# Kernel tuning notes

Hardware: AMD Instinct MI355X
Metric: run time of the kernel (lower is better)

## Reference

```python
import jax, jax.numpy as jnp
import numpy as np

B, L, DM, DI, N = 8, 2048, 512, 768, 8  # batch, seq, d_model, d_inner=int(1.5*512), d_state


def setup_inputs() -> dict:
    key = jax.random.key(0)
    ks = jax.random.split(key, 8)
    g = lambda k, shape, sc=1.0: (jax.random.normal(k, shape, jnp.float32) * sc)
    return {
        "x": g(ks[0], (B, L, DM)),
        "W_in": g(ks[1], (DM, 2 * DI), 0.02),    # in_proj weight (stored in->out)
        "A_log": g(ks[2], (DI, N)),               # nn.Parameter(randn)
        "D_param": g(ks[3], (DI,)),               # skip-connection D
        "W_x": g(ks[4], (DI, N), 0.02),           # x_proj weight
        "W_dt": g(ks[5], (N, DI), 0.02),          # dt_proj weight
        "b_dt": jnp.zeros((DI,), jnp.float32),    # dt_proj bias
        "W_out": g(ks[6], (DI, DM), 0.02),        # out_proj weight
    }


def reference(x, W_in, A_log, D_param, W_x, W_dt, b_dt, W_out):
    xz = x @ W_in                                  # (B,L,2*DI)
    d_inner = W_in.shape[1] // 2
    x_ssm, z = xz[..., :d_inner], xz[..., d_inner:]
    x_ssm = jax.nn.silu(x_ssm)                     # (B,L,DI)
    A = -jnp.exp(A_log.astype(jnp.float32))        # (DI,N)
    delta = jax.nn.softplus((x_ssm @ W_x) @ W_dt + b_dt)  # (B,L,DI)

    n_state = A.shape[-1]

    def step(h, inp):
        xt, dt = inp                               # each (B,DI)
        dA = jnp.exp(dt[..., None] * A)            # (B,DI,N)
        h = dA * h + dt[..., None] * xt[..., None]
        y = jnp.sum(h, axis=-1) + D_param * xt     # (B,DI)
        return h, y

    h0 = jnp.zeros((x.shape[0], d_inner, n_state), x_ssm.dtype)
    xs = (jnp.swapaxes(x_ssm, 0, 1), jnp.swapaxes(delta, 0, 1))  # (L,B,DI)
    _, ys = jax.lax.scan(step, h0, xs)             # ys: (L,B,DI)
    y = jnp.swapaxes(ys, 0, 1)                     # (B,L,DI)
    y = y * jax.nn.silu(z)
    return y @ W_out                               # (B,L,DM)
```

## Files before the change

### kernel.cpp

```cpp
#include <hip/hip_runtime.h>

typedef unsigned short bfu;
typedef __attribute__((ext_vector_type(8))) short short8;
typedef __attribute__((ext_vector_type(4))) float f32x4;

__device__ __forceinline__ float bf2f(bfu u){
  union { unsigned int i; float f; } v; v.i = ((unsigned int)u) << 16; return v.f;
}
__device__ __forceinline__ bfu f2bf(float f){
  union { float f; unsigned int i; } v; v.f = f;
  unsigned int r = (v.i + 0x7FFFu + ((v.i >> 16) & 1u)) >> 16;
  return (bfu)r;
}
__device__ __forceinline__ float fexp2(float x){ return __builtin_amdgcn_exp2f(x); }
__device__ __forceinline__ float flog2(float x){ return __builtin_amdgcn_logf(x); }
__device__ __forceinline__ float softplusf(float x){
  float t = fexp2(-fabsf(x) * 1.44269504088896f);
  return fmaxf(x, 0.f) + 0.69314718055995f * flog2(1.f + t);
}
__device__ __forceinline__ void gload16(const bfu* g, bfu* l){
  __builtin_amdgcn_global_load_lds((const __attribute__((address_space(1))) unsigned int*)g,
                                   (__attribute__((address_space(3))) unsigned int*)l, 16, 0, 0);
}

__global__ __launch_bounds__(256) void cvt_all_kernel(const float* __restrict__ x, bfu* __restrict__ x_bf,
                                                      const float* __restrict__ W_in, const float* __restrict__ W_out,
                                                      const float* __restrict__ W_x,
                                                      bfu* __restrict__ WinT, bfu* __restrict__ WoutT,
                                                      float* __restrict__ WxT){
  int g = blockIdx.x * 256 + threadIdx.x;
  if (g < 2097152){
    float4 v = ((const float4*)x)[g];
    ushort4 o;
    o.x = f2bf(v.x); o.y = f2bf(v.y); o.z = f2bf(v.z); o.w = f2bf(v.w);
    ((ushort4*)x_bf)[g] = o;
    return;
  }
  int h = g - 2097152;
  if (h < 786432){
    int r = h % 512, c = h / 512;
    WinT[h] = f2bf(W_in[(size_t)r * 1536 + c]);
  } else if (h < 786432 + 393216){
    int h2 = h - 786432;
    int r = h2 % 768, c = h2 / 768;
    WoutT[h2] = f2bf(W_out[(size_t)r * 512 + c]);
  } else if (h < 786432 + 393216 + 6144){
    int h2 = h - (786432 + 393216);
    int n = h2 / 768, k = h2 % 768;
    WxT[h2] = W_x[(size_t)k * 8 + n];
  }
}

template<int EPI, int KK>
__global__ __launch_bounds__(512)
void gemm_2p(const bfu* __restrict__ Amat, const bfu* __restrict__ Bt,
             void* __restrict__ out0, void* __restrict__ out1,
             int NBN, int N)
{
  constexpr int NT = KK / 64;
  __shared__ bfu LDS[2 * 24576];
  const int tid  = threadIdx.x;
  const int lane = tid & 63;
  const int w    = tid >> 6;
  const int wr   = w >> 1, wc = w & 1;

  const int cpx = gridDim.x >> 3;
  const int id  = blockIdx.x;
  const int nid = (id & 7) * cpx + (id >> 3);
  const int bn  = nid % NBN;
  const int bm  = nid / NBN;

  const int srow = tid >> 3;
  const int scol = ((tid & 7) ^ (srow & 7)) * 8;
  const bfu* gA = Amat + ((size_t)(bm * 256 + srow)) * KK + scol;
  const bfu* gB = Bt   + ((size_t)(bn * 128 + srow)) * KK + scol;

  auto STAGE = [&](int t, int buf){
    const int k0 = t * 64;
    bfu* dst = (bfu*)LDS + buf * 24576 + tid * 8;
    #pragma unroll
    for (int i = 0; i < 4; i++)
      gload16(gA + (size_t)(i * 64) * KK + k0, dst + i * 4096);
    #pragma unroll
    for (int j = 0; j < 2; j++)
      gload16(gB + (size_t)(j * 64) * KK + k0, dst + 16384 + j * 4096);
  };

  f32x4 acc[4][4];
  #pragma unroll
  for (int i = 0; i < 4; i++)
    #pragma unroll
    for (int j = 0; j < 4; j++)
      #pragma unroll
      for (int r = 0; r < 4; r++) acc[i][j][r] = 0.f;

  STAGE(0, 0);
  asm volatile("s_waitcnt vmcnt(0)" ::: "memory");
  __builtin_amdgcn_s_barrier();

  int cur = 0;
  for (int t = 0; t < NT; ++t){
    if (t + 1 < NT) STAGE(t + 1, cur ^ 1);

    const bfu* Ab = (const bfu*)LDS + cur * 24576;
    const bfu* Bb = Ab + 16384;
    #pragma unroll
    for (int kk = 0; kk < 2; kk++){
      short8 a[4], b[4];
      const int sA = ((kk * 4 + (lane >> 4)) ^ (lane & 7)) * 8;
      #pragma unroll
      for (int m = 0; m < 4; m++){
        int r = wr * 64 + m * 16 + (lane & 15);
        a[m] = *(const short8*)&Ab[r * 64 + sA];
      }
      #pragma unroll
      for (int n = 0; n < 4; n++){
        int r = wc * 64 + n * 16 + (lane & 15);
        b[n] = *(const short8*)&Bb[r * 64 + sA];
      }
      __builtin_amdgcn_s_setprio(1);
      #pragma unroll
      for (int m = 0; m < 4; m++)
        #pragma unroll
        for (int n = 0; n < 4; n++)
          acc[m][n] = __builtin_amdgcn_mfma_f32_16x16x32_bf16(a[m], b[n], acc[m][n], 0, 0, 0);
      __builtin_amdgcn_s_setprio(0);
    }

    if (t + 1 < NT){
      asm volatile("s_waitcnt vmcnt(0)" ::: "memory");
      __builtin_amdgcn_s_barrier();
      cur ^= 1;
    }
  }

  #pragma unroll
  for (int m = 0; m < 4; m++){
    #pragma unroll
    for (int n = 0; n < 4; n++){
      const int row0 = bm * 256 + wr * 64 + m * 16 + (lane >> 4) * 4;
      const int col  = bn * 128 + wc * 64 + n * 16 + (lane & 15);
      #pragma unroll
      for (int r = 0; r < 4; r++){
        float v = acc[m][n][r];
        int row = row0 + r;
        if (EPI == 0){
          float s = v / (1.f + __expf(-v));
          if (col < 768) ((bfu*)out0)[(size_t)row * 768 + col]         = f2bf(s);
          else           ((bfu*)out1)[(size_t)row * 768 + (col - 768)] = f2bf(s);
        } else {
          ((float*)out0)[(size_t)row * N + col] = v;
        }
      }
    }
  }
}

__global__ __launch_bounds__(256) void u_kernel(const bfu* __restrict__ xssm, const float* __restrict__ WxT,
                                                float* __restrict__ u){
  int wid = threadIdx.x >> 6, lane = threadIdx.x & 63;
  int row = blockIdx.x * 4 + wid;
  const bfu* xr = xssm + (size_t)row * 768;
  float acc[8];
  #pragma unroll
  for (int n = 0; n < 8; n++) acc[n] = 0.f;
  #pragma unroll
  for (int i = 0; i < 3; i++){
    int kb = i * 256 + lane * 4;
    ushort4 xq = *(const ushort4*)(xr + kb);
    float x0 = bf2f(xq.x), x1 = bf2f(xq.y), x2 = bf2f(xq.z), x3 = bf2f(xq.w);
    #pragma unroll
    for (int n = 0; n < 8; n++){
      float4 wv = *(const float4*)(WxT + (size_t)n * 768 + kb);
      acc[n] += x0 * wv.x + x1 * wv.y + x2 * wv.z + x3 * wv.w;
    }
  }
  #pragma unroll
  for (int n = 0; n < 8; n++){
    #pragma unroll
    for (int off = 32; off >= 1; off >>= 1) acc[n] += __shfl_xor(acc[n], off, 64);
  }
  if (lane == 0){
    float4 o0 = { acc[0], acc[1], acc[2], acc[3] };
    float4 o1 = { acc[4], acc[5], acc[6], acc[7] };
    *(float4*)(u + (size_t)row * 8)     = o0;
    *(float4*)(u + (size_t)row * 8 + 4) = o1;
  }
}

__global__ __launch_bounds__(128) void scan_phase1(const bfu* __restrict__ xssm, const float* __restrict__ u,
    const float* __restrict__ Wdt, const float* __restrict__ bdt, const float* __restrict__ A_log,
    float* __restrict__ Pws, float* __restrict__ Hws){
  int tid = threadIdx.x;
  int bid = blockIdx.x;
  int b = bid / 192; int rem = bid % 192;
  int c = rem / 3;   int dblk = rem % 3;
  int d0 = dblk * 256 + tid * 2;
  float Al2[2][8], H[2][8], Wr[2][8], bd[2], S[2];
  #pragma unroll
  for (int j = 0; j < 2; j++){
    bd[j] = bdt[d0 + j];
    S[j] = 0.f;
    #pragma unroll
    for (int n = 0; n < 8; n++){
      Al2[j][n] = -__expf(A_log[(size_t)(d0 + j) * 8 + n]) * 1.4426950408889634f;
      Wr[j][n]  = Wdt[(size_t)n * 768 + d0 + j];
      H[j][n] = 0.f;
    }
  }
  int r0 = b * 2048 + c * 32;
  size_t base = (size_t)r0 * 768 + d0;
  #pragma unroll 8
  for (int i = 0; i < 32; i++){
    float4 u0 = *(const float4*)(u + (size_t)(r0 + i) * 8);
    float4 u1 = *(const float4*)(u + (size_t)(r0 + i) * 8 + 4);
    ushort2 xq = *(const ushort2*)(xssm + base + (size_t)i * 768);
    #pragma unroll
    for (int j = 0; j < 2; j++){
      float xt = bf2f(j == 0 ? xq.x : xq.y);
      float dv = bd[j] + u0.x * Wr[j][0] + u0.y * Wr[j][1] + u0.z * Wr[j][2] + u0.w * Wr[j][3]
                       + u1.x * Wr[j][4] + u1.y * Wr[j][5] + u1.z * Wr[j][6] + u1.w * Wr[j][7];
      float dt = softplusf(dv);
      float dx = dt * xt;
      S[j] += dt;
      #pragma unroll
      for (int n = 0; n < 8; n++){
        float e = fexp2(dt * Al2[j][n]);
        H[j][n] = e * H[j][n] + dx;
      }
    }
  }
  size_t o = (((size_t)b * 64 + c) * 768 + d0) * 8;
  #pragma unroll
  for (int j = 0; j < 2; j++){
    float4 p0, p1;
    p0.x = fexp2(S[j] * Al2[j][0]); p0.y = fexp2(S[j] * Al2[j][1]);
    p0.z = fexp2(S[j] * Al2[j][2]); p0.w = fexp2(S[j] * Al2[j][3]);
    p1.x = fexp2(S[j] * Al2[j][4]); p1.y = fexp2(S[j] * Al2[j][5]);
    p1.z = fexp2(S[j] * Al2[j][6]); p1.w = fexp2(S[j] * Al2[j][7]);
    float4 h0 = { H[j][0], H[j][1], H[j][2], H[j][3] };
    float4 h1 = { H[j][4], H[j][5], H[j][6], H[j][7] };
    *(float4*)(Pws + o + j * 8)     = p0;
    *(float4*)(Pws + o + j * 8 + 4) = p1;
    *(float4*)(Hws + o + j * 8)     = h0;
    *(float4*)(Hws + o + j * 8 + 4) = h1;
  }
}

__global__ __launch_bounds__(256) void scan_phase2(float* __restrict__ Pws, const float* __restrict__ Hws){
  int g = blockIdx.x * 256 + threadIdx.x;
  int within = g % 6144;
  int b = g / 6144;
  size_t base = (size_t)b * 64 * 6144 + within;
  float hin = 0.f;
  #pragma unroll 8
  for (int c = 0; c < 64; c++){
    size_t idx = base + (size_t)c * 6144;
    float p = Pws[idx], hh = Hws[idx];
    Pws[idx] = hin;
    hin = p * hin + hh;
  }
}

__global__ __launch_bounds__(128) void scan_phase3(const bfu* __restrict__ xssm, const float* __restrict__ u,
    const float* __restrict__ Wdt, const float* __restrict__ bdt, const float* __restrict__ A_log,
    const float* __restrict__ Dp, const bfu* __restrict__ siluz, const float* __restrict__ Hin,
    bfu* __restrict__ yz){
  int tid = threadIdx.x;
  int bid = blockIdx.x;
  int b = bid / 192; int rem = bid % 192;
  int c = rem / 3;   int dblk = rem % 3;
  int d0 = dblk * 256 + tid * 2;
  float Al2[2][8], H[2][8], Wr[2][8], bd[2], Dd[2];
  size_t o = (((size_t)b * 64 + c) * 768 + d0) * 8;
  #pragma unroll
  for (int j = 0; j < 2; j++){
    bd[j] = bdt[d0 + j];
    Dd[j] = Dp[d0 + j];
    float4 h0 = *(const float4*)(Hin + o + j * 8);
    float4 h1 = *(const float4*)(Hin + o + j * 8 + 4);
    H[j][0] = h0.x; H[j][1] = h0.y; H[j][2] = h0.z; H[j][3] = h0.w;
    H[j][4] = h1.x; H[j][5] = h1.y; H[j][6] = h1.z; H[j][7] = h1.w;
    #pragma unroll
    for (int n = 0; n < 8; n++){
      Al2[j][n] = -__expf(A_log[(size_t)(d0 + j) * 8 + n]) * 1.4426950408889634f;
      Wr[j][n]  = Wdt[(size_t)n * 768 + d0 + j];
    }
  }
  int r0 = b * 2048 + c * 32;
  size_t base = (size_t)r0 * 768 + d0;
  #pragma unroll 8
  for (int i = 0; i < 32; i++){
    float4 u0 = *(const float4*)(u + (size_t)(r0 + i) * 8);
    float4 u1 = *(const float4*)(u + (size_t)(r0 + i) * 8 + 4);
    ushort2 xq = *(const ushort2*)(xssm + base + (size_t)i * 768);
    ushort2 zq = *(const ushort2*)(siluz + base + (size_t)i * 768);
    ushort2 oq;
    #pragma unroll
    for (int j = 0; j < 2; j++){
      float xt = bf2f(j == 0 ? xq.x : xq.y);
      float dv = bd[j] + u0.x * Wr[j][0] + u0.y * Wr[j][1] + u0.z * Wr[j][2] + u0.w * Wr[j][3]
                       + u1.x * Wr[j][4] + u1.y * Wr[j][5] + u1.z * Wr[j][6] + u1.w * Wr[j][7];
      float dt = softplusf(dv);
      float dx = dt * xt;
      float y = Dd[j] * xt;
      #pragma unroll
      for (int n = 0; n < 8; n++){
        float e = fexp2(dt * Al2[j][n]);
        H[j][n] = e * H[j][n] + dx;
        y += H[j][n];
      }
      float sz = bf2f(j == 0 ? zq.x : zq.y);
      bfu r = f2bf(y * sz);
      if (j == 0) oq.x = r; else oq.y = r;
    }
    *(ushort2*)(yz + base + (size_t)i * 768) = oq;
  }
}

extern "C" void kernel_launch(void* const* d_in, const int* in_sizes, int n_in,
                              void* d_out, int out_size, void* d_ws, size_t ws_size,
                              hipStream_t stream){
  const float* x     = (const float*)d_in[0];
  const float* W_in  = (const float*)d_in[1];
  const float* A_log = (const float*)d_in[2];
  const float* D_par = (const float*)d_in[3];
  const float* W_x   = (const float*)d_in[4];
  const float* W_dt  = (const float*)d_in[5];
  const float* b_dt  = (const float*)d_in[6];
  const float* W_out = (const float*)d_in[7];
  float* out = (float*)d_out;
  (void)in_sizes; (void)n_in; (void)out_size; (void)ws_size;

  char* base = (char*)d_ws;
  size_t off = 0;
  auto alloc = [&](size_t bytes)->char*{
    char* p = base + off; off += (bytes + 255) & ~(size_t)255; return p;
  };
  bfu*   x_bf  = (bfu*)  alloc((size_t)16384 * 512 * 2);
  bfu*   WinT  = (bfu*)  alloc((size_t)1536 * 512 * 2);
  bfu*   WoutT = (bfu*)  alloc((size_t)512 * 768 * 2);
  float* WxT   = (float*)alloc((size_t)8 * 768 * 4);
  bfu*   xssm  = (bfu*)  alloc((size_t)16384 * 768 * 2);
  bfu*   siluz = (bfu*)  alloc((size_t)16384 * 768 * 2);
  float* u     = (float*)alloc((size_t)16384 * 8 * 4);
  float* Pws   = (float*)alloc((size_t)8 * 64 * 768 * 8 * 4);
  float* Hws   = (float*)alloc((size_t)8 * 64 * 768 * 8 * 4);
  bfu*   yz    = (bfu*)  alloc((size_t)16384 * 768 * 2);

  cvt_all_kernel<<<12824, 256, 0, stream>>>(x, x_bf, W_in, W_out, W_x, WinT, WoutT, WxT);
  gemm_2p<0, 512><<<768, 512, 0, stream>>>(x_bf, WinT, xssm, siluz, 12, 1536);
  u_kernel<<<4096, 256, 0, stream>>>(xssm, WxT, u);
  scan_phase1<<<1536, 128, 0, stream>>>(xssm, u, W_dt, b_dt, A_log, Pws, Hws);
  scan_phase2<<<192, 256, 0, stream>>>(Pws, Hws);
  scan_phase3<<<1536, 128, 0, stream>>>(xssm, u, W_dt, b_dt, A_log, D_par, siluz, Pws, yz);
  gemm_2p<1, 768><<<256, 512, 0, stream>>>(yz, WoutT, out, nullptr, 4, 512);
}
```

Before: 165.8 us.

## Fuse fp32-to-bf16 conversion of x into the input projection GEMM

Removes the separate conversion pass over x and has the first GEMM load fp32 activations into registers, convert them to bf16 and store them into swizzled LDS while the B tile streams via direct global-to-LDS loads. This eliminates writing and rereading a bf16 copy of x and one launch. In exchange, each column block rereads fp32 A (twice the bytes) and the conversion adds VALU work and register pressure to the GEMM main loop. The setprio hints around the MFMA block in the output GEMM are also dropped.

```diff
diff --git a/kernel.cpp b/kernel.cpp
--- a/kernel.cpp
+++ b/kernel.cpp
@@ -23,20 +23,11 @@
                                    (__attribute__((address_space(3))) unsigned int*)l, 16, 0, 0);
 }
 
-__global__ __launch_bounds__(256) void cvt_all_kernel(const float* __restrict__ x, bfu* __restrict__ x_bf,
-                                                      const float* __restrict__ W_in, const float* __restrict__ W_out,
-                                                      const float* __restrict__ W_x,
-                                                      bfu* __restrict__ WinT, bfu* __restrict__ WoutT,
-                                                      float* __restrict__ WxT){
-  int g = blockIdx.x * 256 + threadIdx.x;
-  if (g < 2097152){
-    float4 v = ((const float4*)x)[g];
-    ushort4 o;
-    o.x = f2bf(v.x); o.y = f2bf(v.y); o.z = f2bf(v.z); o.w = f2bf(v.w);
-    ((ushort4*)x_bf)[g] = o;
-    return;
-  }
-  int h = g - 2097152;
+__global__ __launch_bounds__(256) void cvt_w_kernel(const float* __restrict__ W_in, const float* __restrict__ W_out,
+                                                    const float* __restrict__ W_x,
+                                                    bfu* __restrict__ WinT, bfu* __restrict__ WoutT,
+                                                    float* __restrict__ WxT){
+  int h = blockIdx.x * 256 + threadIdx.x;
   if (h < 786432){
     int r = h % 512, c = h / 512;
     WinT[h] = f2bf(W_in[(size_t)r * 1536 + c]);
@@ -51,11 +42,138 @@
   }
 }
 
-template<int EPI, int KK>
+__global__ __launch_bounds__(512)
+void gemm_f1(const float* __restrict__ x, const bfu* __restrict__ Bt,
+             bfu* __restrict__ out0, bfu* __restrict__ out1, int NBN)
+{
+  constexpr int KK = 512;
+  constexpr int NT = KK / 64;
+  __shared__ bfu LDS[2 * 24576];
+  const int tid  = threadIdx.x;
+  const int lane = tid & 63;
+  const int w    = tid >> 6;
+  const int wr   = w >> 1, wc = w & 1;
+
+  const int cpx = gridDim.x >> 3;
+  const int id  = blockIdx.x;
+  const int nid = (id & 7) * cpx + (id >> 3);
+  const int bn  = nid % NBN;
+  const int bm  = nid / NBN;
+
+  const int arow = tid >> 3;
+  const int aslot = tid & 7;
+  const float* gx = x + ((size_t)(bm * 256 + arow)) * 512 + aslot * 8;
+  const int wslot = (aslot ^ (arow & 7)) * 8;
+
+  const int srow = tid >> 3;
+  const int scol = ((tid & 7) ^ (srow & 7)) * 8;
+  const bfu* gB = Bt + ((size_t)(bn * 128 + srow)) * KK + scol;
+
+  float4 av[4][2];
+  auto ALOAD = [&](int t){
+    const int k0 = t * 64;
+    #pragma unroll
+    for (int p = 0; p < 4; p++){
+      const float* src = gx + (size_t)(p * 64) * 512 + k0;
+      av[p][0] = *(const float4*)src;
+      av[p][1] = *(const float4*)(src + 4);
+    }
+  };
+  auto ACVT = [&](int buf){
+    bfu* dst = (bfu*)LDS + buf * 24576;
+    #pragma unroll
+    for (int p = 0; p < 4; p++){
+      short8 pk;
+      pk[0] = (short)f2bf(av[p][0].x); pk[1] = (short)f2bf(av[p][0].y);
+      pk[2] = (short)f2bf(av[p][0].z); pk[3] = (short)f2bf(av[p][0].w);
+      pk[4] = (short)f2bf(av[p][1].x); pk[5] = (short)f2bf(av[p][1].y);
+      pk[6] = (short)f2bf(av[p][1].z); pk[7] = (short)f2bf(av[p][1].w);
+      *(short8*)&dst[(p * 64 + arow) * 64 + wslot] = pk;
+    }
+  };
+  auto STAGE_B = [&](int t, int buf){
+    const int k0 = t * 64;
+    bfu* dst = (bfu*)LDS + buf * 24576 + 16384 + tid * 8;
+    #pragma unroll
+    for (int j = 0; j < 2; j++)
+      gload16(gB + (size_t)(j * 64) * KK + k0, dst + j * 4096);
+  };
+
+  f32x4 acc[4][4];
+  #pragma unroll
+  for (int i = 0; i < 4; i++)
+    #pragma unroll
+    for (int j = 0; j < 4; j++)
+      #pragma unroll
+      for (int r = 0; r < 4; r++) acc[i][j][r] = 0.f;
+
+  ALOAD(0);
+  STAGE_B(0, 0);
+  ACVT(0);
+  asm volatile("s_waitcnt vmcnt(0) lgkmcnt(0)" ::: "memory");
+  __builtin_amdgcn_s_barrier();
+
+  int cur = 0;
+  for (int t = 0; t < NT; ++t){
+    if (t + 1 < NT){
+      ALOAD(t + 1);
+      STAGE_B(t + 1, cur ^ 1);
+      __builtin_amdgcn_sched_barrier(0);
+    }
+
+    const bfu* Ab = (const bfu*)LDS + cur * 24576;
+    const bfu* Bb = Ab + 16384;
+    #pragma unroll
+    for (int kk = 0; kk < 2; kk++){
+      short8 a[4], b[4];
+      const int sA = ((kk * 4 + (lane >> 4)) ^ (lane & 7)) * 8;
+      #pragma unroll
+      for (int m = 0; m < 4; m++){
+        int r = wr * 64 + m * 16 + (lane & 15);
+        a[m] = *(const short8*)&Ab[r * 64 + sA];
+      }
+      #pragma unroll
+      for (int n = 0; n < 4; n++){
+        int r = wc * 64 + n * 16 + (lane & 15);
+        b[n] = *(const short8*)&Bb[r * 64 + sA];
+      }
+      #pragma unroll
+      for (int m = 0; m < 4; m++)
+        #pragma unroll
+        for (int n = 0; n < 4; n++)
+          acc[m][n] = __builtin_amdgcn_mfma_f32_16x16x32_bf16(a[m], b[n], acc[m][n], 0, 0, 0);
+    }
+
+    if (t + 1 < NT){
+      ACVT(cur ^ 1);
+      asm volatile("s_waitcnt vmcnt(0) lgkmcnt(0)" ::: "memory");
+      __builtin_amdgcn_s_barrier();
+      cur ^= 1;
+    }
+  }
+
+  #pragma unroll
+  for (int m = 0; m < 4; m++){
+    #pragma unroll
+    for (int n = 0; n < 4; n++){
+      const int row0 = bm * 256 + wr * 64 + m * 16 + (lane >> 4) * 4;
+      const int col  = bn * 128 + wc * 64 + n * 16 + (lane & 15);
+      #pragma unroll
+      for (int r = 0; r < 4; r++){
+        float v = acc[m][n][r];
+        int row = row0 + r;
+        float s = v / (1.f + __expf(-v));
+        if (col < 768) out0[(size_t)row * 768 + col]         = f2bf(s);
+        else           out1[(size_t)row * 768 + (col - 768)] = f2bf(s);
+      }
+    }
+  }
+}
+
+template<int KK>
 __global__ __launch_bounds__(512)
 void gemm_2p(const bfu* __restrict__ Amat, const bfu* __restrict__ Bt,
-             void* __restrict__ out0, void* __restrict__ out1,
-             int NBN, int N)
+             float* __restrict__ out0, int NBN, int N)
 {
   constexpr int NT = KK / 64;
   __shared__ bfu LDS[2 * 24576];
@@ -118,13 +236,11 @@
         int r = wc * 64 + n * 16 + (lane & 15);
         b[n] = *(const short8*)&Bb[r * 64 + sA];
       }
-      __builtin_amdgcn_s_setprio(1);
       #pragma unroll
       for (int m = 0; m < 4; m++)
         #pragma unroll
         for (int n = 0; n < 4; n++)
           acc[m][n] = __builtin_amdgcn_mfma_f32_16x16x32_bf16(a[m], b[n], acc[m][n], 0, 0, 0);
-      __builtin_amdgcn_s_setprio(0);
     }
 
     if (t + 1 < NT){
@@ -141,17 +257,8 @@
       const int row0 = bm * 256 + wr * 64 + m * 16 + (lane >> 4) * 4;
       const int col  = bn * 128 + wc * 64 + n * 16 + (lane & 15);
       #pragma unroll
-      for (int r = 0; r < 4; r++){
-        float v = acc[m][n][r];
-        int row = row0 + r;
-        if (EPI == 0){
-          float s = v / (1.f + __expf(-v));
-          if (col < 768) ((bfu*)out0)[(size_t)row * 768 + col]         = f2bf(s);
-          else           ((bfu*)out1)[(size_t)row * 768 + (col - 768)] = f2bf(s);
-        } else {
-          ((float*)out0)[(size_t)row * N + col] = v;
-        }
-      }
+      for (int r = 0; r < 4; r++)
+        out0[(size_t)(row0 + r) * N + col] = acc[m][n][r];
     }
   }
 }
@@ -337,7 +444,6 @@
   auto alloc = [&](size_t bytes)->char*{
     char* p = base + off; off += (bytes + 255) & ~(size_t)255; return p;
   };
-  bfu*   x_bf  = (bfu*)  alloc((size_t)16384 * 512 * 2);
   bfu*   WinT  = (bfu*)  alloc((size_t)1536 * 512 * 2);
   bfu*   WoutT = (bfu*)  alloc((size_t)512 * 768 * 2);
   float* WxT   = (float*)alloc((size_t)8 * 768 * 4);
@@ -348,11 +454,11 @@
   float* Hws   = (float*)alloc((size_t)8 * 64 * 768 * 8 * 4);
   bfu*   yz    = (bfu*)  alloc((size_t)16384 * 768 * 2);
 
-  cvt_all_kernel<<<12824, 256, 0, stream>>>(x, x_bf, W_in, W_out, W_x, WinT, WoutT, WxT);
-  gemm_2p<0, 512><<<768, 512, 0, stream>>>(x_bf, WinT, xssm, siluz, 12, 1536);
+  cvt_w_kernel<<<4632, 256, 0, stream>>>(W_in, W_out, W_x, WinT, WoutT, WxT);
+  gemm_f1<<<768, 512, 0, stream>>>(x, WinT, xssm, siluz, 12);
   u_kernel<<<4096, 256, 0, stream>>>(xssm, WxT, u);
   scan_phase1<<<1536, 128, 0, stream>>>(xssm, u, W_dt, b_dt, A_log, Pws, Hws);
   scan_phase2<<<192, 256, 0, stream>>>(Pws, Hws);
   scan_phase3<<<1536, 128, 0, stream>>>(xssm, u, W_dt, b_dt, A_log, D_par, siluz, Pws, yz);
-  gemm_2p<1, 768><<<256, 512, 0, stream>>>(yz, WoutT, out, nullptr, 4, 512);
-}
+  gemm_2p<768><<<256, 512, 0, stream>>>(yz, WoutT, out, 4, 512);
+}
```

Result: slower. 180.5 us (+8.9%).
